# Performance work log

Measured on AMD Instinct MI355X. Metric: run time of the kernel, lower is better.

The kernel has to match this reference:

```python
import jax, jax.numpy as jnp
import numpy as np

EPS = 1e-6
HID = 2048; N_HEADS = 16; Q_LORA = 768; KV_LORA = 512
ROPE_D = 64; NOPE_D = 128; V_D = 128
IDX_H = 32; IDX_D = 128; IDX_TOPK = 512
N_EXP = 8; TOPK = 4; N_GROUP = 4; TOPK_GROUP = 2
MOE_I = 512; SHARED_I = 512; ROUTED_SCALE = 2.5
T = 1024
NEG = -1e30


def _rms(x, w, eps=EPS):
    x = x.astype(jnp.float32)
    return x * jax.lax.rsqrt(jnp.mean(x * x, axis=-1, keepdims=True) + eps) * w


def _ln(x, w, b, eps=EPS):
    x = x.astype(jnp.float32)
    m = jnp.mean(x, axis=-1, keepdims=True)
    v = jnp.mean((x - m) ** 2, axis=-1, keepdims=True)
    return (x - m) * jax.lax.rsqrt(v + eps) * w + b


def _rope_cs(positions, dim):
    inv = 1.0 / (10000.0 ** (jnp.arange(0, dim, 2, dtype=jnp.float32) / dim))
    f = positions.astype(jnp.float32)[:, None] * inv[None, :]  # [T, dim/2]
    return jnp.cos(f), jnp.sin(f)


def _rope(x, cos, sin):
    # neox-style rotate-half over last dim
    d = x.shape[-1] // 2
    x1, x2 = x[..., :d], x[..., d:]
    while cos.ndim < x.ndim:
        cos, sin = cos[:, None], sin[:, None]
    return jnp.concatenate([x1 * cos - x2 * sin, x2 * cos + x1 * sin], axis=-1)


def setup_inputs() -> dict:
    key = jax.random.key(0)
    ks = iter(jax.random.split(key, 32))
    w = lambda *s: jax.random.normal(next(ks), s, jnp.float32) * 0.02
    inp = {
        'positions': jnp.arange(T, dtype=jnp.int32),
        'hidden_states': jax.random.normal(next(ks), (T, HID), jnp.float32),
        'residual': jax.random.normal(next(ks), (T, HID), jnp.float32),
        'w_input_ln': jnp.ones((HID,), jnp.float32),
        'w_post_ln': jnp.ones((HID,), jnp.float32),
        'w_step1': w(Q_LORA + KV_LORA + ROPE_D + IDX_D + IDX_H, HID),
        'w_q_a_ln': jnp.ones((Q_LORA,), jnp.float32),
        'w_kv_a_ln': jnp.ones((KV_LORA,), jnp.float32),
        'idx_k_ln_w': jnp.ones((IDX_D,), jnp.float32),
        'idx_k_ln_b': jnp.zeros((IDX_D,), jnp.float32),
        'w_step3': w(IDX_H * IDX_D + N_HEADS * (NOPE_D + ROPE_D), Q_LORA),
        'W_UK_T': w(N_HEADS, NOPE_D, KV_LORA),
        'W_UV': w(N_HEADS, KV_LORA, V_D),
        'w_o': w(HID, N_HEADS * V_D),
        'gate_w': w(N_EXP, HID),
        'gate_bias': jnp.zeros((N_EXP,), jnp.float32),
        'shared_gate_up': w(2 * SHARED_I, HID),
        'shared_down': w(HID, SHARED_I),
        'exp_gate_up': w(N_EXP, 2 * MOE_I, HID),
        'exp_down': w(N_EXP, HID, MOE_I),
    }
    return inp


def reference(positions, hidden_states, residual, w_input_ln, w_post_ln, w_step1,
              w_q_a_ln, w_kv_a_ln, idx_k_ln_w, idx_k_ln_b, w_step3, W_UK_T, W_UV,
              w_o, gate_w, gate_bias, shared_gate_up, shared_down, exp_gate_up, exp_down):
    Tn = hidden_states.shape[0]
    rows = jnp.arange(Tn)
    # (allreduce is identity at tp=1) + residual add + RMSNorm
    res = hidden_states.astype(jnp.float32) + residual.astype(jnp.float32)
    h = _rms(res, w_input_ln)
    # ---- Step 1: fused qkv_a + indexer_wk + indexer_weights_proj GEMM ----
    s1 = h @ w_step1.T
    o0 = 0
    q_c = s1[:, o0:o0 + Q_LORA]; o0 += Q_LORA
    kv_c = s1[:, o0:o0 + KV_LORA]; o0 += KV_LORA
    k_pe = s1[:, o0:o0 + ROPE_D]; o0 += ROPE_D
    idx_k = s1[:, o0:o0 + IDX_D]; o0 += IDX_D
    idx_w_raw = s1[:, o0:o0 + IDX_H]
    cos, sin = _rope_cs(positions, ROPE_D)
    # fused_norm_rope: norms + rope on k_pe / indexer-k
    q_c = _rms(q_c, w_q_a_ln)
    kv_c = _rms(kv_c, w_kv_a_ln)
    k_pe = _rope(k_pe, cos, sin)
    idx_k = _ln(idx_k, idx_k_ln_w, idx_k_ln_b)
    idx_k = jnp.concatenate([_rope(idx_k[:, :ROPE_D], cos, sin), idx_k[:, ROPE_D:]], axis=-1)
    # ---- Step 3: fused indexer_wq_b + q_b_proj GEMM ----
    s3 = q_c @ w_step3.T
    idx_q = s3[:, :IDX_H * IDX_D].reshape(Tn, IDX_H, IDX_D)
    q = s3[:, IDX_H * IDX_D:].reshape(Tn, N_HEADS, NOPE_D + ROPE_D)
    q_nope, q_pe = q[..., :NOPE_D], q[..., NOPE_D:]
    # absorb W_UK: [T,H,nope] x [H,nope,kv_lora] -> [T,H,kv_lora]
    ql_nope = jnp.einsum('thn,hnk->thk', q_nope, W_UK_T)
    q_pe = _rope(q_pe, cos, sin)
    idx_q = jnp.concatenate([_rope(idx_q[..., :ROPE_D], cos, sin), idx_q[..., ROPE_D:]], axis=-1)
    idx_q = idx_q * (IDX_D ** -0.5)            # indexer softmax scale
    idx_w = idx_w_raw * (IDX_H ** -0.5)        # per-head weights scale
    # ---- sparse attention indexer: relu(q.k) head-weighted sum, causal top-k ----
    il = jnp.einsum('thd,sd->ths', idx_q, idx_k)          # [T,Hi,S]
    iscores = jnp.einsum('ths,th->ts', jax.nn.relu(il), idx_w)
    causal = positions[:, None] >= positions[None, :]
    iscores = jnp.where(causal, iscores, NEG)
    topk_idx = jax.lax.top_k(iscores, IDX_TOPK)[1]        # [T, IDX_TOPK]
    tmask = jnp.zeros((Tn, Tn), bool).at[rows[:, None], topk_idx].set(True)
    mask = causal & tmask
    # ---- MLA MQA attention in latent space ----
    mqa_q = jnp.concatenate([ql_nope, jnp.broadcast_to(q_pe, (Tn, N_HEADS, ROPE_D))], axis=-1)
    kv = jnp.concatenate([kv_c, k_pe], axis=-1)           # [S, kv_lora+rope]
    att = jnp.einsum('thd,sd->hts', mqa_q, kv) * ((NOPE_D + ROPE_D) ** -0.5)
    att = jnp.where(mask[None], att, NEG)
    p = jax.nn.softmax(att, axis=-1)
    o = jnp.einsum('hts,sk->thk', p, kv_c)                # [T,H,kv_lora]
    o = jnp.einsum('thk,hkv->thv', o, W_UV).reshape(Tn, N_HEADS * V_D)
    attn_out = o @ w_o.T
    # add + RMSNorm
    res2 = attn_out + res
    h2 = _rms(res2, w_post_ln)
    # ---- MoE: DeepSeekV3 sigmoid grouped routing + shared experts ----
    glog = h2 @ gate_w.T
    sg = jax.nn.sigmoid(glog)
    sc = sg + gate_bias
    gsz = N_EXP // N_GROUP
    grp = sc.reshape(Tn, N_GROUP, gsz)
    grp_score = jax.lax.top_k(grp, min(2, gsz))[0].sum(-1)
    gidx = jax.lax.top_k(grp_score, TOPK_GROUP)[1]
    gmask = jnp.zeros((Tn, N_GROUP), bool).at[rows[:, None], gidx].set(True)
    emask = jnp.repeat(gmask, gsz, axis=1)
    sc_m = jnp.where(emask, sc, NEG)
    _, tid = jax.lax.top_k(sc_m, TOPK)
    tw = jnp.take_along_axis(sg, tid, axis=1)
    tw = tw / (tw.sum(-1, keepdims=True) + 1e-20) * ROUTED_SCALE
    comb = jnp.zeros((Tn, N_EXP), jnp.float32).at[rows[:, None], tid].set(tw)
    # routed experts (dense masked combine as reference for grouped-GEMM dispatch)
    gu = jnp.einsum('th,eih->tei', h2, exp_gate_up)       # [T,E,2I]
    act = jax.nn.silu(gu[..., :MOE_I]) * gu[..., MOE_I:]
    routed_e = jnp.einsum('tei,ehi->teh', act, exp_down)  # [T,E,H]
    routed = jnp.einsum('te,teh->th', comb, routed_e)
    # shared experts
    gus = h2 @ shared_gate_up.T
    shared = (jax.nn.silu(gus[:, :SHARED_I]) * gus[:, SHARED_I:]) @ shared_down.T
    out = shared + routed
    return out, res2
```

## Files before the change

### kernel.cpp

```cpp
#include <hip/hip_runtime.h>
#include <math.h>

static constexpr int TT  = 1024;
static constexpr int HID = 2048;
static constexpr int NH  = 16;
static constexpr int QL  = 768;
static constexpr int KVL = 512;
static constexpr int RD  = 64;
static constexpr int IH  = 32;
static constexpr int ID  = 128;
static constexpr int S1W = QL + KVL + RD + ID + IH;
static constexpr int S3W = IH*ID + NH*(128+RD);

#define SCALE_ATT 0.07216878364870323f
#define SC_IDXQ   0.08838834764831845f
#define SC_IDXW   0.17677669529663687f
#define NEGR      -1e30f
#define NEGL      -3.0e38f

typedef __bf16 bf16x8 __attribute__((ext_vector_type(8)));
typedef float  f32x4  __attribute__((ext_vector_type(4)));

#define GLD_LDS16(g, l) __builtin_amdgcn_global_load_lds( \
    (const __attribute__((address_space(1))) void*)(g),   \
    (__attribute__((address_space(3))) void*)(l), 16, 0, 0)

__device__ __forceinline__ unsigned short f2b(float x) {
  union { float f; unsigned u; } v; v.f = x;
  unsigned r = v.u + 0x7FFFu + ((v.u >> 16) & 1u);
  return (unsigned short)(r >> 16);
}
__device__ __forceinline__ float b2f(unsigned short u) {
  union { unsigned u; float f; } v; v.u = ((unsigned)u) << 16;
  return v.f;
}

__device__ __forceinline__ float blk_sum256(float v, float* s) {
  #pragma unroll
  for (int o = 32; o > 0; o >>= 1) v += __shfl_down(v, o, 64);
  __syncthreads();
  if ((threadIdx.x & 63) == 0) s[threadIdx.x >> 6] = v;
  __syncthreads();
  return s[0] + s[1] + s[2] + s[3];
}

__global__ __launch_bounds__(256) void k_prelude(const float* __restrict__ hs,
                                                 const float* __restrict__ rsd,
                                                 const float* __restrict__ w,
                                                 float* __restrict__ res,
                                                 unsigned short* __restrict__ hb) {
  int t = blockIdx.x;
  __shared__ float scr[4];
  float vals[8]; float ss = 0.f;
  #pragma unroll
  for (int r = 0; r < 8; r++) {
    int d = threadIdx.x + 256*r;
    float v = hs[(size_t)t*HID + d] + rsd[(size_t)t*HID + d];
    vals[r] = v; res[(size_t)t*HID + d] = v; ss = fmaf(v, v, ss);
  }
  ss = blk_sum256(ss, scr);
  float inv = 1.f/sqrtf(ss/(float)HID + 1e-6f);
  #pragma unroll
  for (int r = 0; r < 8; r++) {
    int d = threadIdx.x + 256*r;
    hb[(size_t)t*HID + d] = f2b(vals[r]*inv*w[d]);
  }
}

__global__ __launch_bounds__(256) void k_res2(const float* __restrict__ attn1,
                                              const float* __restrict__ attn2,
                                              const float* __restrict__ res,
                                              const float* __restrict__ w,
                                              float* __restrict__ res2_out,
                                              float* __restrict__ h2,
                                              unsigned short* __restrict__ h2b) {
  int t = blockIdx.x;
  __shared__ float scr[4];
  float vals[8]; float ss = 0.f;
  #pragma unroll
  for (int r = 0; r < 8; r++) {
    int d = threadIdx.x + 256*r;
    float v = attn1[(size_t)t*HID + d] + attn2[(size_t)t*HID + d] + res[(size_t)t*HID + d];
    vals[r] = v; res2_out[(size_t)t*HID + d] = v; ss = fmaf(v, v, ss);
  }
  ss = blk_sum256(ss, scr);
  float inv = 1.f/sqrtf(ss/(float)HID + 1e-6f);
  #pragma unroll
  for (int r = 0; r < 8; r++) {
    int d = threadIdx.x + 256*r;
    float o = vals[r]*inv*w[d];
    h2[(size_t)t*HID + d] = o;
    h2b[(size_t)t*HID + d] = f2b(o);
  }
}

__global__ void k_ropecs(const int* __restrict__ pos, float* __restrict__ cosb, float* __restrict__ sinb) {
  int i = blockIdx.x*256 + threadIdx.x;
  if (i >= TT*32) return;
  int t = i >> 5, k = i & 31;
  double inv = pow(10000.0, -((double)(2*k))/64.0);
  double f = (double)pos[t] * inv;
  cosb[i] = (float)cos(f);
  sinb[i] = (float)sin(f);
}

__global__ void k_f2b(const float* __restrict__ s, unsigned short* __restrict__ d,
                      long long n, long long ntot) {
  long long stride = (long long)gridDim.x * 1024;
  for (long long i = ((long long)blockIdx.x*256 + threadIdx.x)*4; i < ntot; i += stride) {
    float x0, x1, x2, x3;
    if (i + 3 < n) { float4 v = *(const float4*)(s + i); x0=v.x; x1=v.y; x2=v.z; x3=v.w; }
    else {
      x0 = (i   < n) ? s[i]   : 0.f; x1 = (i+1 < n) ? s[i+1] : 0.f;
      x2 = (i+2 < n) ? s[i+2] : 0.f; x3 = (i+3 < n) ? s[i+3] : 0.f;
    }
    ushort4 o; o.x=f2b(x0); o.y=f2b(x1); o.z=f2b(x2); o.w=f2b(x3);
    *(ushort4*)(d + i) = o;
  }
}

__global__ void k_f2b4(const float* __restrict__ s0, unsigned short* __restrict__ d0, long long n0,
                       const float* __restrict__ s1, unsigned short* __restrict__ d1, long long n1,
                       const float* __restrict__ s2, unsigned short* __restrict__ d2, long long n2,
                       const float* __restrict__ s3, unsigned short* __restrict__ d3, long long n3) {
  long long ntot = n0 + n1 + n2 + n3;
  long long stride = (long long)gridDim.x * 1024;
  for (long long i = ((long long)blockIdx.x*256 + threadIdx.x)*4; i < ntot; i += stride) {
    const float* s; unsigned short* d; long long j = i;
    if (j < n0) { s = s0; d = d0; }
    else { j -= n0;
      if (j < n1) { s = s1; d = d1; }
      else { j -= n1;
        if (j < n2) { s = s2; d = d2; }
        else { j -= n2; s = s3; d = d3; } } }
    float4 v = *(const float4*)(s + j);
    ushort4 o; o.x=f2b(v.x); o.y=f2b(v.y); o.z=f2b(v.z); o.w=f2b(v.w);
    *(ushort4*)(d + j) = o;
  }
}

__global__ __launch_bounds__(256) void k_tconvb(const float* __restrict__ src,
                                                unsigned short* __restrict__ dst,
                                                int R, int C) {
  src += (size_t)blockIdx.z * R * C;
  dst += (size_t)blockIdx.z * R * C;
  __shared__ float tile[32][33];
  int c0 = blockIdx.x * 32, r0 = blockIdx.y * 32;
  int tx = threadIdx.x & 31, ty = threadIdx.x >> 5;
  #pragma unroll
  for (int i = 0; i < 4; i++) {
    int r = r0 + ty + i*8;
    tile[ty + i*8][tx] = src[(size_t)r*C + c0 + tx];
  }
  __syncthreads();
  #pragma unroll
  for (int i = 0; i < 4; i++) {
    int c = c0 + ty + i*8;
    dst[(size_t)c*R + r0 + tx] = f2b(tile[tx][ty + i*8]);
  }
}

template<int BM, int OUT, bool ILV, int MOE>
__global__ __launch_bounds__(256) void k_mgemm(
    const unsigned short* __restrict__ A, int lda, long long sA,
    const unsigned short* __restrict__ B, int ldb, long long sB,
    void* __restrict__ Cv, int ldc, long long sC,
    int N, int K, float alpha, int cskip, int ktri,
    int nseg, long long segA, long long segB,
    const float* __restrict__ comb,
    const int* __restrict__ cntp, const int* __restrict__ tokp) {
  constexpr int MR  = BM / 32;
  constexpr int ITA = BM / 32;
  const int row0 = blockIdx.y * BM;
  const int col0 = blockIdx.x * 128;
  const int tid  = threadIdx.x;
  if (cskip >= 0 && col0 > row0 + cskip) {
    if (OUT == 3) {
      float* C = (float*)Cv;
      for (int i = tid; i < BM*32; i += 256) {
        int rr = i >> 5, cc = (i & 31) * 4;
        float4 ng = make_float4(NEGR, NEGR, NEGR, NEGR);
        *(float4*)&C[(size_t)(row0 + rr)*ldc + col0 + cc] = ng;
      }
    }
    return;
  }
  const int zb = blockIdx.z;
  int cnt = 0; long long off = 0;
  if (MOE) {
    cnt = cntp[zb];
    for (int e = 0; e < zb; e++) off += cntp[e];
    if (row0 >= cnt) return;
  }
  __shared__ __align__(16) unsigned short As[2][BM*64];
  __shared__ __align__(16) unsigned short Bs[2][128*64];
  __shared__ float wlds[(OUT == 3) ? BM*32 : 1];
  const int wave = tid >> 6, lane = tid & 63;
  const int wm = wave >> 1, wn = wave & 1;
  A += (size_t)zb * (size_t)sA;
  B += (size_t)zb * (size_t)sB;
  if (MOE == 2) A += off * (long long)lda;

  if constexpr (OUT == 3) {
    for (int i = tid; i < BM*32; i += 256)
      wlds[i] = comb[(size_t)(row0 + (i >> 5))*32 + (i & 31)];
  }

  int tki[ITA];
  if (MOE == 1) {
    #pragma unroll
    for (int it = 0; it < ITA; it++) {
      int r = (wave*64 + it*256 + lane) >> 3;
      tki[it] = tokp[zb*1024 + row0 + r];
    }
  }

  f32x4 acc[MR][4] = {};
  f32x4 acc2[(OUT == 3) ? MR : 1][4] = {};
  const int l15 = lane & 15, l4 = lane >> 4;
  const int sx = l15 & 7;
  int Kend = K;
  if (ktri) {
    int kub = (((row0 + BM - 1) >> 7) + 1) << 7;
    if (kub < Kend) Kend = kub;
  }
  const int nk = Kend >> 6;
  const int nt = nseg * nk;

  auto STAGE = [&](int b, const unsigned short* Ab, const unsigned short* Bb, int k0) {
    #pragma unroll
    for (int it = 0; it < ITA; it++) {
      int base = wave*64 + it*256;
      int sidx = base + lane;
      int r = sidx >> 3, s = sidx & 7;
      int s_src = s ^ (r & 7);
      const unsigned short* ga;
      if (MOE == 1) ga = Ab + (size_t)tki[it]*lda + k0 + s_src*8;
      else          ga = Ab + (size_t)(row0 + r)*lda + k0 + s_src*8;
      GLD_LDS16(ga, &As[b][base*8]);
    }
    #pragma unroll
    for (int it = 0; it < 4; it++) {
      int base = wave*64 + it*256;
      int sidx = base + lane;
      int r = sidx >> 3, s = sidx & 7;
      int s_src = s ^ (r & 7);
      int rt = col0 + r;
      int srow = ILV ? ((rt >> 1) + (rt & 1)*512) : rt;
      const unsigned short* gb = Bb + (size_t)srow*ldb + k0 + s_src*8;
      GLD_LDS16(gb, &Bs[b][base*8]);
    }
  };

  STAGE(0, A, B, 0);
  int ks = 64, sg = 0;
  if (ks == Kend) { ks = 0; sg = 1; }
  __syncthreads();
  int cur = 0;

  for (int u = 0; u < nt; u++) {
    if (u + 1 < nt) {
      STAGE(cur ^ 1, A + (size_t)sg*segA, B + (size_t)sg*segB, ks);
      ks += 64;
      if (ks == Kend) { ks = 0; sg++; }
    }
    #pragma unroll
    for (int kc = 0; kc < 2; kc++) {
      const int sl = ((kc*4 + l4) ^ sx) << 3;
      bf16x8 fa[MR], fb[4];
      #pragma unroll
      for (int mf = 0; mf < MR; mf++)
        fa[mf] = *(const bf16x8*)&As[cur][(wm*(BM/2) + mf*16 + l15)*64 + sl];
      #pragma unroll
      for (int nf = 0; nf < 4; nf++)
        fb[nf] = *(const bf16x8*)&Bs[cur][(wn*64 + nf*16 + l15)*64 + sl];
      #pragma unroll
      for (int mf = 0; mf < MR; mf++)
        #pragma unroll
        for (int nf = 0; nf < 4; nf++)
          acc[mf][nf] = __builtin_amdgcn_mfma_f32_16x16x32_bf16(fa[mf], fb[nf], acc[mf][nf], 0, 0, 0);
    }
    if constexpr (OUT == 3) {
      if ((u + 1) % nk == 0) {
        int h = u / nk;
        #pragma unroll
        for (int mf = 0; mf < MR; mf++) {
          #pragma unroll
          for (int r = 0; r < 4; r++) {
            int rl = wm*(BM/2) + mf*16 + l4*4 + r;
            float w = wlds[rl*32 + h];
            #pragma unroll
            for (int nf = 0; nf < 4; nf++) {
              acc2[mf][nf][r] += fmaxf(acc[mf][nf][r], 0.f) * w;
              acc[mf][nf][r] = 0.f;
            }
          }
        }
      }
    }
    __syncthreads();
    cur ^= 1;
  }

  #pragma unroll
  for (int mf = 0; mf < MR; mf++) {
    #pragma unroll
    for (int nf = 0; nf < 4; nf++) {
      int n = col0 + wn*64 + nf*16 + l15;
      #pragma unroll
      for (int r = 0; r < 4; r++) {
        int m = row0 + wm*(BM/2) + mf*16 + l4*4 + r;
        if (OUT == 3) {
          float v = acc2[mf][nf][r];
          if (n > 512 + m) v = NEGR;
          ((float*)Cv)[(size_t)m*ldc + n] = v;
          continue;
        }
        float v = acc[mf][nf][r] * alpha;
        if (OUT == 2) {
          float p = __shfl_xor(v, 1, 64);
          if ((l15 & 1) == 0) {
            bool ok = true;
            long long mrow = m;
            float w;
            if (MOE == 1) {
              ok = (m < cnt); mrow = off + m;
              int tok = tokp[zb*1024 + m];
              w = (zb < 8) ? comb[tok*8 + zb] : 1.f;
            } else {
              w = (zb < 8) ? comb[m*8 + zb] : 1.f;
            }
            if (ok) {
              float rres = v/(1.f + expf(-v)) * p * w;
              ((unsigned short*)Cv)[(size_t)zb*sC + (size_t)mrow*ldc + (n >> 1)] = f2b(rres);
            }
          }
        } else if (n < N) {
          bool ok = true;
          long long mrow = m;
          if (MOE == 2) { ok = (m < cnt); mrow = off + m; }
          if (ok) {
            size_t idx = (size_t)mrow*ldc + n;
            if (OUT == 1) ((unsigned short*)Cv)[(size_t)zb*sC + idx] = f2b(v);
            else          ((float*)Cv)[(size_t)zb*sC + idx] = v;
          }
        }
      }
    }
  }
}

__global__ __launch_bounds__(256) void k_post1(const float* __restrict__ s1a,
    const float* __restrict__ s1b,
    const float* __restrict__ wq, const float* __restrict__ wkv,
    const float* __restrict__ lnw, const float* __restrict__ lnb,
    const float* __restrict__ cosb, const float* __restrict__ sinb,
    unsigned short* __restrict__ qcb, float* __restrict__ kvc, float* __restrict__ kpe,
    float* __restrict__ idxk, float* __restrict__ idxw) {
  int t = blockIdx.x, tid = threadIdx.x;
  __shared__ float rowb[S1W];
  __shared__ float scr[4];
  __shared__ float yb[128];
  for (int d = tid; d < S1W; d += 256)
    rowb[d] = s1a[(size_t)t*S1W + d] + s1b[(size_t)t*S1W + d];
  __syncthreads();
  float ss = 0.f;
  for (int d = tid; d < QL; d += 256) { float v = rowb[d]; ss = fmaf(v,v,ss); }
  ss = blk_sum256(ss, scr);
  float inv = 1.f/sqrtf(ss/(float)QL + 1e-6f);
  for (int d = tid; d < QL; d += 256) qcb[(size_t)t*QL + d] = f2b(rowb[d]*inv*wq[d]);
  ss = 0.f;
  for (int d = tid; d < KVL; d += 256) { float v = rowb[QL+d]; ss = fmaf(v,v,ss); }
  ss = blk_sum256(ss, scr);
  inv = 1.f/sqrtf(ss/(float)KVL + 1e-6f);
  for (int d = tid; d < KVL; d += 256) kvc[(size_t)t*KVL + d] = rowb[QL+d]*inv*wkv[d];
  float sm = (tid < 128) ? rowb[1344 + tid] : 0.f;
  float tot = blk_sum256(sm, scr);
  float mean = tot / 128.f;
  float vs = 0.f;
  if (tid < 128) { float v = rowb[1344+tid] - mean; vs = v*v; }
  vs = blk_sum256(vs, scr);
  float ivn = 1.f/sqrtf(vs/128.f + 1e-6f);
  if (tid < 128) yb[tid] = (rowb[1344+tid]-mean)*ivn*lnw[tid] + lnb[tid];
  __syncthreads();
  if (tid < 32) {
    float c = cosb[t*32 + tid], s = sinb[t*32 + tid];
    idxk[(size_t)t*ID + tid]      = yb[tid]*c - yb[32+tid]*s;
    idxk[(size_t)t*ID + 32 + tid] = yb[32+tid]*c + yb[tid]*s;
    float x1 = rowb[1280+tid], x2 = rowb[1312+tid];
    kpe[(size_t)t*RD + tid]      = x1*c - x2*s;
    kpe[(size_t)t*RD + 32 + tid] = x2*c + x1*s;
    idxw[(size_t)t*IH + tid] = rowb[1472+tid] * SC_IDXW;
  } else if (tid >= 64 && tid < 128) {
    idxk[(size_t)t*ID + tid] = yb[tid];
  }
}

__global__ __launch_bounds__(256) void k_post3b(const float* __restrict__ s3,
                                                const float* __restrict__ cosb,
                                                const float* __restrict__ sinb,
                                                unsigned short* __restrict__ s3b) {
  int t = blockIdx.x, tid = threadIdx.x;
  const float* row = s3 + (size_t)t*S3W;
  __shared__ float buf[S3W];
  __shared__ float cs[32], sn[32];
  if (tid < 32) { cs[tid] = cosb[t*32+tid]; sn[tid] = sinb[t*32+tid]; }
  for (int d = tid; d < S3W; d += 256) buf[d] = row[d];
  __syncthreads();
  for (int p = tid; p < 1024; p += 256) {
    int h = p >> 5, d = p & 31;
    float c = cs[d], s = sn[d];
    float x1 = buf[h*ID + d], x2 = buf[h*ID + 32 + d];
    buf[h*ID + d]      = (x1*c - x2*s) * SC_IDXQ;
    buf[h*ID + 32 + d] = (x2*c + x1*s) * SC_IDXQ;
  }
  for (int p = tid; p < 2048; p += 256) {
    int h = p >> 6, d = 64 + (p & 63);
    buf[h*ID + d] *= SC_IDXQ;
  }
  for (int p = tid; p < 512; p += 256) {
    int h = p >> 5, d = p & 31;
    float c = cs[d], s = sn[d];
    int base = IH*ID + h*192 + 128;
    float x1 = buf[base + d], x2 = buf[base + 32 + d];
    buf[base + d]      = x1*c - x2*s;
    buf[base + 32 + d] = x2*c + x1*s;
  }
  __syncthreads();
  unsigned short* orow = s3b + (size_t)t*S3W;
  for (int g = tid*4; g < S3W; g += 1024) {
    ushort4 o;
    o.x = f2b(buf[g]); o.y = f2b(buf[g+1]); o.z = f2b(buf[g+2]); o.w = f2b(buf[g+3]);
    *(ushort4*)(orow + g) = o;
  }
}

__global__ void k_qpe(const unsigned short* __restrict__ s3b, unsigned short* __restrict__ qm) {
  int i = blockIdx.x*256 + threadIdx.x;
  int t = i >> 10, r = i & 1023;
  int h = r >> 6, j = r & 63;
  float v = b2f(s3b[(size_t)t*S3W + IH*ID + h*192 + 128 + j]) * SCALE_ATT;
  qm[(size_t)t*9216 + h*576 + 512 + j] = f2b(v);
}

__global__ void k_kvb(const float* __restrict__ kvc, const float* __restrict__ kpe,
                      unsigned short* __restrict__ kvb) {
  int i = blockIdx.x*256 + threadIdx.x;
  int s = i / 576, d = i - s*576;
  float v = (d < 512) ? kvc[(size_t)s*KVL + d] : kpe[(size_t)s*RD + (d - 512)];
  kvb[i] = f2b(v);
}

__global__ __launch_bounds__(512) void k_topk(const float* __restrict__ isc,
                                              unsigned char* __restrict__ mask) {
  int t = 512 + blockIdx.x;
  const float* row = isc + (size_t)blockIdx.x * TT;
  __shared__ unsigned long long keys[1024];
  int tid = threadIdx.x;
  for (int i = tid; i < 1024; i += 512) {
    float v = row[i];
    unsigned int b = __float_as_uint(v);
    unsigned int u = (b & 0x80000000u) ? ~b : (b | 0x80000000u);
    keys[i] = ((unsigned long long)u << 32) | (unsigned int)(1023 - i);
  }
  __syncthreads();
  for (int k = 2; k <= 1024; k <<= 1) {
    for (int j = k >> 1; j > 0; j >>= 1) {
      int i = ((tid & ~(j - 1)) << 1) | (tid & (j - 1));
      int l = i | j;
      unsigned long long a = keys[i], b = keys[l];
      bool up = ((i & k) == 0);
      if ((a < b) == up) { keys[i] = b; keys[l] = a; }
      __syncthreads();
    }
  }
  unsigned char* mrow = mask + (size_t)t * TT;
  for (int p = tid; p < 1024; p += 512) {
    int s = 1023 - (int)(keys[p] & 0xFFFFFFFFu);
    mrow[s] = (p < 512) ? (unsigned char)1 : (unsigned char)0;
  }
}

__global__ __launch_bounds__(256) void k_psoft(unsigned short* __restrict__ pb,
                                               const unsigned char* __restrict__ mask) {
  int b = blockIdx.x;
  int t = b & 1023, h = b >> 10;
  unsigned short* row = pb + ((size_t)h << 20) + ((size_t)t << 10);
  int tid = threadIdx.x;
  __shared__ float scr[4];
  int s0 = tid * 4;
  int rub = ((t >> 7) + 1) << 7;
  bool act = (s0 < rub);
  float v0 = 0.f, v1 = 0.f, v2 = 0.f, v3 = 0.f;
  bool m0 = false, m1 = false, m2 = false, m3 = false;
  if (act) {
    ushort4 raw = *(const ushort4*)(row + s0);
    v0 = b2f(raw.x); v1 = b2f(raw.y); v2 = b2f(raw.z); v3 = b2f(raw.w);
    if (t < 512) {
      m0 = (s0 <= t); m1 = (s0+1 <= t); m2 = (s0+2 <= t); m3 = (s0+3 <= t);
    } else {
      uchar4 mk = *(const uchar4*)(mask + (size_t)t*TT + s0);
      m0 = (s0 <= t) && mk.x; m1 = (s0+1 <= t) && mk.y;
      m2 = (s0+2 <= t) && mk.z; m3 = (s0+3 <= t) && mk.w;
    }
  }
  float mx = NEGL;
  if (m0) mx = v0;
  if (m1) mx = fmaxf(mx, v1);
  if (m2) mx = fmaxf(mx, v2);
  if (m3) mx = fmaxf(mx, v3);
  #pragma unroll
  for (int o = 32; o > 0; o >>= 1) mx = fmaxf(mx, __shfl_down(mx, o, 64));
  __syncthreads();
  if ((tid & 63) == 0) scr[tid >> 6] = mx;
  __syncthreads();
  mx = fmaxf(fmaxf(scr[0], scr[1]), fmaxf(scr[2], scr[3]));
  float p0 = m0 ? expf(v0 - mx) : 0.f;
  float p1 = m1 ? expf(v1 - mx) : 0.f;
  float p2 = m2 ? expf(v2 - mx) : 0.f;
  float p3 = m3 ? expf(v3 - mx) : 0.f;
  float sum = blk_sum256((p0+p1)+(p2+p3), scr);
  float inv = 1.f / sum;
  if (act) {
    ushort4 o;
    o.x = f2b(p0*inv); o.y = f2b(p1*inv); o.z = f2b(p2*inv); o.w = f2b(p3*inv);
    *(ushort4*)(row + s0) = o;
  }
}

__global__ __launch_bounds__(256) void k_gate(const float* __restrict__ h2,
                                              const float* __restrict__ gw,
                                              const float* __restrict__ gb,
                                              float* __restrict__ comb) {
  int t = blockIdx.x, tid = threadIdx.x;
  int e = tid >> 5, lane = tid & 31;
  __shared__ float gl[8];
  float p = 0.f;
  for (int d = lane; d < HID; d += 32) p = fmaf(h2[(size_t)t*HID+d], gw[(size_t)e*HID+d], p);
  #pragma unroll
  for (int o = 16; o > 0; o >>= 1) p += __shfl_down(p, o, 32);
  if (lane == 0) gl[e] = p;
  __syncthreads();
  if (tid == 0) {
    float sg[8], sc[8];
    #pragma unroll
    for (int i = 0; i < 8; i++) { sg[i] = 1.f/(1.f+expf(-gl[i])); sc[i] = sg[i] + gb[i]; }
    float gs[4];
    #pragma unroll
    for (int g = 0; g < 4; g++) gs[g] = sc[2*g] + sc[2*g+1];
    int g0 = 0;
    for (int g = 1; g < 4; g++) if (gs[g] > gs[g0]) g0 = g;
    int g1 = -1;
    for (int g = 0; g < 4; g++) { if (g == g0) continue; if (g1 < 0 || gs[g] > gs[g1]) g1 = g; }
    float wsum = 1e-20f;
    #pragma unroll
    for (int i = 0; i < 8; i++) { int g = i >> 1; if (g == g0 || g == g1) wsum += sg[i]; }
    #pragma unroll
    for (int i = 0; i < 8; i++) { int g = i >> 1; comb[t*8+i] = (g == g0 || g == g1) ? sg[i]/wsum*2.5f : 0.f; }
  }
}

__global__ __launch_bounds__(1024) void k_route(const float* __restrict__ comb,
                                                int* __restrict__ tokidx,
                                                int* __restrict__ rank,
                                                int* __restrict__ cntp) {
  int e = blockIdx.x;
  int t = threadIdx.x;
  if (e == 8) {
    tokidx[8*1024 + t] = t;
    if (t == 0) cntp[8] = 1024;
    return;
  }
  int lane = t & 63, w = t >> 6;
  bool sel = comb[t*8 + e] != 0.0f;
  unsigned long long bal = __ballot(sel);
  int pw = __popcll(bal & ((1ull << lane) - 1ull));
  int wt = __popcll(bal);
  __shared__ int wsum[16];
  if (lane == 0) wsum[w] = wt;
  __syncthreads();
  int woff = 0, total = 0;
  #pragma unroll
  for (int i = 0; i < 16; i++) { int v = wsum[i]; if (i < w) woff += v; total += v; }
  int pos = woff + pw;
  rank[t*8 + e] = sel ? pos : -1;
  if (sel) tokidx[e*1024 + pos] = t;
  __syncthreads();
  if (t >= total) tokidx[e*1024 + t] = 0;
  if (t == 0) cntp[e] = total;
}

__global__ __launch_bounds__(256) void k_rsum(const unsigned short* __restrict__ dpc,
                                              const int* __restrict__ rank,
                                              const int* __restrict__ cntp,
                                              float* __restrict__ out) {
  int t = blockIdx.x;
  int d = threadIdx.x * 8;
  int offs[8]; int acc_off = 0;
  #pragma unroll
  for (int e = 0; e < 8; e++) { offs[e] = acc_off; acc_off += cntp[e]; }
  const unsigned short* ps = dpc + (size_t)(acc_off + t)*2048 + d;
  ushort4 u0 = *(const ushort4*)ps;
  ushort4 u1 = *(const ushort4*)(ps + 4);
  float a[8];
  a[0]=b2f(u0.x); a[1]=b2f(u0.y); a[2]=b2f(u0.z); a[3]=b2f(u0.w);
  a[4]=b2f(u1.x); a[5]=b2f(u1.y); a[6]=b2f(u1.z); a[7]=b2f(u1.w);
  #pragma unroll
  for (int e = 0; e < 8; e++) {
    int r = rank[t*8 + e];
    if (r >= 0) {
      const unsigned short* p = dpc + (size_t)(offs[e] + r)*2048 + d;
      ushort4 b0 = *(const ushort4*)p;
      ushort4 b1 = *(const ushort4*)(p + 4);
      a[0]+=b2f(b0.x); a[1]+=b2f(b0.y); a[2]+=b2f(b0.z); a[3]+=b2f(b0.w);
      a[4]+=b2f(b1.x); a[5]+=b2f(b1.y); a[6]+=b2f(b1.z); a[7]+=b2f(b1.w);
    }
  }
  float* po = out + (size_t)t*2048 + d;
  *(float4*)po       = make_float4(a[0], a[1], a[2], a[3]);
  *(float4*)(po + 4) = make_float4(a[4], a[5], a[6], a[7]);
}

extern "C" void kernel_launch(void* const* d_in, const int* in_sizes, int n_in,
                              void* d_out, int out_size, void* d_ws, size_t ws_size,
                              hipStream_t stream) {
  const int*   positions = (const int*)d_in[0];
  const float* hs     = (const float*)d_in[1];
  const float* rsd    = (const float*)d_in[2];
  const float* w_in   = (const float*)d_in[3];
  const float* w_post = (const float*)d_in[4];
  const float* w_s1   = (const float*)d_in[5];
  const float* w_qln  = (const float*)d_in[6];
  const float* w_kvln = (const float*)d_in[7];
  const float* iklnw  = (const float*)d_in[8];
  const float* iklnb  = (const float*)d_in[9];
  const float* w_s3   = (const float*)d_in[10];
  const float* wukt   = (const float*)d_in[11];
  const float* wuv    = (const float*)d_in[12];
  const float* w_o    = (const float*)d_in[13];
  const float* gate_w = (const float*)d_in[14];
  const float* gate_b = (const float*)d_in[15];
  const float* sh_gu  = (const float*)d_in[16];
  const float* sh_dn  = (const float*)d_in[17];
  const float* ex_gu  = (const float*)d_in[18];
  const float* ex_dn  = (const float*)d_in[19];

  float* ws = (float*)d_ws;
  typedef unsigned short ush;
  float* RES   = ws + 0;
  float* COSB  = ws + 2097152;
  float* SINB  = ws + 2129920;
  float* KVC   = ws + 2162688;
  float* KPE   = ws + 2686976;
  float* IDXK  = ws + 2752512;
  float* IDXW  = ws + 2883584;
  float* COMB  = ws + 2916352;
  ush*   HB    = (ush*)(ws + 2924544);
  ush*   WS1B  = (ush*)(ws + 3973120);
  float* S1P0  = ws + 5545984;
  ush*   QCB   = (ush*)(ws + 7086080);
  ush*   WS3B  = (ush*)(ws + 7479296);
  ush*   WOB   = (ush*)(ws + 7479296);
  float* S3    = ws + 10231808;
  float* S1P1  = ws + 10231808;
  ush*   S3B   = (ush*)(ws + 17571840);
  ush*   WUKTB = (ush*)(ws + 21241856);
  ush*   QMQAB = (ush*)(ws + 21766144);
  float* ISC   = ws + 26484736;
  unsigned char* MASK = (unsigned char*)(ws + 27009024);
  ush*   WUVB  = (ush*)(ws + 27271168);
  ush*   KVB   = (ush*)(ws + 27795456);
  ush*   VTB   = (ush*)(ws + 28090368);
  ush*   O2B   = (ush*)(ws + 28352512);
  ush*   IDXKB = (ush*)(ws + 31989760);
  ush*   PB    = (ush*)(ws + 10231808);
  ush*   OHB   = (ush*)(ws + 18620416);
  float* ATTNP = ws + 10231808;
  float* H2     = ws + 2924544;
  ush*   H2B    = (ush*)(ws + 5021696);
  ush*   EXGUB  = (ush*)(ws + 6070272);
  ush*   SHGUB  = (ush*)(ws + 14458880);
  ush*   EXDNB  = (ush*)(ws + 15507456);
  ush*   SHDNB  = (ush*)(ws + 19701760);
  ush*   ACTC   = (ush*)(ws + 20226048);
  ush*   DPC    = (ush*)(ws + 21536768);
  int*   TOKIDX = (int*)(ws + 32022528);
  int*   RANK   = (int*)(ws + 32031744);
  int*   CNT    = (int*)(ws + 32039936);

  float* OUT0 = (float*)d_out;
  float* OUT_RES2 = OUT0 + (size_t)TT*HID;

  k_prelude<<<TT, 256, 0, stream>>>(hs, rsd, w_in, RES, HB);
  k_ropecs<<<(TT*32)/256, 256, 0, stream>>>(positions, COSB, SINB);
  k_f2b<<<1024, 256, 0, stream>>>(w_s1, WS1B, 3080192LL, 3145728LL);
  k_f2b<<<1024, 256, 0, stream>>>(w_s3, WS3B, 5505024LL, 5505024LL);
  k_tconvb<<<dim3(16,4,16), 256, 0, stream>>>(wukt, WUKTB, 128, 512);
  k_tconvb<<<dim3(4,16,16), 256, 0, stream>>>(wuv, WUVB, 512, 128);
  k_mgemm<128,0,false,0><<<dim3(12,8,2), 256, 0, stream>>>(
      HB, 2048, 1024, WS1B, 2048, 1024, S1P0, S1W, 4685824,
      1504, 1024, 1.f, -1, 0, 1, 0, 0, nullptr, nullptr, nullptr);
  k_post1<<<TT, 256, 0, stream>>>(S1P0, S1P1, w_qln, w_kvln, iklnw, iklnb, COSB, SINB, QCB, KVC, KPE, IDXK, IDXW);
  k_f2b<<<128, 256, 0, stream>>>(IDXK, IDXKB, 131072LL, 131072LL);
  k_mgemm<128,0,false,0><<<dim3(56,8,1), 256, 0, stream>>>(
      QCB, 768, 0, WS3B, 768, 0, S3, S3W, 0,
      S3W, 768, 1.f, -1, 0, 1, 0, 0, nullptr, nullptr, nullptr);
  k_post3b<<<TT, 256, 0, stream>>>(S3, COSB, SINB, (ush*)S3B);
  k_f2b<<<1024, 256, 0, stream>>>(w_o, WOB, 4194304LL, 4194304LL);
  k_mgemm<128,1,false,0><<<dim3(4,8,16), 256, 0, stream>>>(
      S3B + 4096, S3W, 192, WUKTB, 128, 65536, QMQAB, 9216, 576,
      512, 128, SCALE_ATT, -1, 0, 1, 0, 0, nullptr, nullptr, nullptr);
  k_qpe<<<4096, 256, 0, stream>>>(S3B, QMQAB);
  k_mgemm<64,3,false,0><<<dim3(8,8,1), 256, 0, stream>>>(
      S3B + (size_t)512*S3W, S3W, 0, IDXKB, 128, 0,
      ISC, 1024, 0, 1024, 128, 1.f, 575, 0, 32, 128, 0,
      IDXW + (size_t)512*IH, nullptr, nullptr);
  k_topk<<<512, 512, 0, stream>>>(ISC, MASK);
  k_kvb<<<2304, 256, 0, stream>>>(KVC, KPE, KVB);
  k_tconvb<<<dim3(16,32,1), 256, 0, stream>>>(KVC, VTB, 1024, 512);
  k_mgemm<128,1,false,0><<<dim3(8,8,16), 256, 0, stream>>>(
      QMQAB, 9216, 576, KVB, 576, 0, PB, 1024, 1048576,
      1024, 576, 1.f, 127, 0, 1, 0, 0, nullptr, nullptr, nullptr);
  k_psoft<<<16384, 256, 0, stream>>>(PB, MASK);
  k_mgemm<128,1,false,0><<<dim3(4,8,16), 256, 0, stream>>>(
      PB, 1024, 1048576, VTB, 1024, 0, OHB, 512, 524288,
      512, 1024, 1.f, -1, 1, 1, 0, 0, nullptr, nullptr, nullptr);
  k_mgemm<128,1,false,0><<<dim3(1,8,16), 256, 0, stream>>>(
      OHB, 512, 524288, WUVB, 512, 65536, O2B, 2048, 128,
      128, 512, 1.f, -1, 0, 1, 0, 0, nullptr, nullptr, nullptr);
  k_mgemm<128,0,false,0><<<dim3(16,8,2), 256, 0, stream>>>(
      O2B, 2048, 1024, WOB, 2048, 1024, ATTNP, 2048, 2097152,
      2048, 1024, 1.f, -1, 0, 1, 0, 0, nullptr, nullptr, nullptr);
  k_res2<<<TT, 256, 0, stream>>>(ATTNP, ATTNP + 2097152, RES, w_post, OUT_RES2, H2, H2B);
  k_gate<<<TT, 256, 0, stream>>>(H2, gate_w, gate_b, COMB);
  k_route<<<9, 1024, 0, stream>>>(COMB, TOKIDX, RANK, CNT);
  k_f2b4<<<2048, 256, 0, stream>>>(ex_gu, EXGUB, 16777216LL,
                                   sh_gu, SHGUB, 2097152LL,
                                   ex_dn, EXDNB, 8388608LL,
                                   sh_dn, SHDNB, 1048576LL);
  k_mgemm<128,2,true,1><<<dim3(8,8,9), 256, 0, stream>>>(
      H2B, 2048, 0, EXGUB, 2048, 2097152, ACTC, 512, 0,
      1024, 2048, 1.f, -1, 0, 1, 0, 0, COMB, CNT, TOKIDX);
  k_mgemm<128,1,false,2><<<dim3(16,8,9), 256, 0, stream>>>(
      ACTC, 512, 0, EXDNB, 512, 1048576, DPC, 2048, 0,
      2048, 512, 1.f, -1, 0, 1, 0, 0, nullptr, CNT, nullptr);
  k_rsum<<<TT, 256, 0, stream>>>(DPC, RANK, CNT, OUT0);
}
```

Baseline: 426.9 us.

## Deepen GEMM prefetch pipeline and fuse bf16 pack kernels into post-processing

```diff
diff --git a/kernel.cpp b/kernel.cpp
--- a/kernel.cpp
+++ b/kernel.cpp
@@ -24,6 +24,22 @@
 #define GLD_LDS16(g, l) __builtin_amdgcn_global_load_lds( \
     (const __attribute__((address_space(1))) void*)(g),   \
     (__attribute__((address_space(3))) void*)(l), 16, 0, 0)
+
+__device__ __forceinline__ void pipe_barrier() {
+  __builtin_amdgcn_sched_barrier(0);
+  asm volatile("" ::: "memory");
+  __builtin_amdgcn_s_barrier();
+  asm volatile("" ::: "memory");
+  __builtin_amdgcn_sched_barrier(0);
+}
+__device__ __forceinline__ void wait_vm8() {
+  asm volatile("s_waitcnt vmcnt(8)" ::: "memory");
+  __builtin_amdgcn_sched_barrier(0);
+}
+__device__ __forceinline__ void wait_vm0() {
+  asm volatile("s_waitcnt vmcnt(0)" ::: "memory");
+  __builtin_amdgcn_sched_barrier(0);
+}
 
 __device__ __forceinline__ unsigned short f2b(float x) {
   union { float f; unsigned u; } v; v.f = x;
@@ -254,16 +270,18 @@
 
   STAGE(0, A, B, 0);
   int ks = 64, sg = 0;
-  if (ks == Kend) { ks = 0; sg = 1; }
-  __syncthreads();
-  int cur = 0;
+  if (ks == Kend) { ks = 0; sg++; }
+  if (nt > 1) {
+    STAGE(1, A + (size_t)sg*segA, B + (size_t)sg*segB, ks);
+    ks += 64; if (ks == Kend) { ks = 0; sg++; }
+    wait_vm8();
+  } else {
+    wait_vm0();
+  }
+  pipe_barrier();
 
   for (int u = 0; u < nt; u++) {
-    if (u + 1 < nt) {
-      STAGE(cur ^ 1, A + (size_t)sg*segA, B + (size_t)sg*segB, ks);
-      ks += 64;
-      if (ks == Kend) { ks = 0; sg++; }
-    }
+    const int cur = u & 1;
     #pragma unroll
     for (int kc = 0; kc < 2; kc++) {
       const int sl = ((kc*4 + l4) ^ sx) << 3;
@@ -298,8 +316,17 @@
         }
       }
     }
-    __syncthreads();
-    cur ^= 1;
+    pipe_barrier();
+    if (u + 1 < nt) {
+      if (u + 2 < nt) {
+        STAGE(cur, A + (size_t)sg*segA, B + (size_t)sg*segB, ks);
+        ks += 64; if (ks == Kend) { ks = 0; sg++; }
+        wait_vm8();
+      } else {
+        wait_vm0();
+      }
+      pipe_barrier();
+    }
   }
 
   #pragma unroll
@@ -355,8 +382,9 @@
     const float* __restrict__ wq, const float* __restrict__ wkv,
     const float* __restrict__ lnw, const float* __restrict__ lnb,
     const float* __restrict__ cosb, const float* __restrict__ sinb,
-    unsigned short* __restrict__ qcb, float* __restrict__ kvc, float* __restrict__ kpe,
-    float* __restrict__ idxk, float* __restrict__ idxw) {
+    unsigned short* __restrict__ qcb, float* __restrict__ kvc,
+    unsigned short* __restrict__ kvb, unsigned short* __restrict__ idxkb,
+    float* __restrict__ idxw) {
   int t = blockIdx.x, tid = threadIdx.x;
   __shared__ float rowb[S1W];
   __shared__ float scr[4];
@@ -373,7 +401,11 @@
   for (int d = tid; d < KVL; d += 256) { float v = rowb[QL+d]; ss = fmaf(v,v,ss); }
   ss = blk_sum256(ss, scr);
   inv = 1.f/sqrtf(ss/(float)KVL + 1e-6f);
-  for (int d = tid; d < KVL; d += 256) kvc[(size_t)t*KVL + d] = rowb[QL+d]*inv*wkv[d];
+  for (int d = tid; d < KVL; d += 256) {
+    float v = rowb[QL+d]*inv*wkv[d];
+    kvc[(size_t)t*KVL + d] = v;
+    kvb[(size_t)t*576 + d] = f2b(v);
+  }
   float sm = (tid < 128) ? rowb[1344 + tid] : 0.f;
   float tot = blk_sum256(sm, scr);
   float mean = tot / 128.f;
@@ -385,21 +417,22 @@
   __syncthreads();
   if (tid < 32) {
     float c = cosb[t*32 + tid], s = sinb[t*32 + tid];
-    idxk[(size_t)t*ID + tid]      = yb[tid]*c - yb[32+tid]*s;
-    idxk[(size_t)t*ID + 32 + tid] = yb[32+tid]*c + yb[tid]*s;
+    idxkb[(size_t)t*ID + tid]      = f2b(yb[tid]*c - yb[32+tid]*s);
+    idxkb[(size_t)t*ID + 32 + tid] = f2b(yb[32+tid]*c + yb[tid]*s);
     float x1 = rowb[1280+tid], x2 = rowb[1312+tid];
-    kpe[(size_t)t*RD + tid]      = x1*c - x2*s;
-    kpe[(size_t)t*RD + 32 + tid] = x2*c + x1*s;
+    kvb[(size_t)t*576 + 512 + tid] = f2b(x1*c - x2*s);
+    kvb[(size_t)t*576 + 544 + tid] = f2b(x2*c + x1*s);
     idxw[(size_t)t*IH + tid] = rowb[1472+tid] * SC_IDXW;
   } else if (tid >= 64 && tid < 128) {
-    idxk[(size_t)t*ID + tid] = yb[tid];
+    idxkb[(size_t)t*ID + tid] = f2b(yb[tid]);
   }
 }
 
 __global__ __launch_bounds__(256) void k_post3b(const float* __restrict__ s3,
                                                 const float* __restrict__ cosb,
                                                 const float* __restrict__ sinb,
-                                                unsigned short* __restrict__ s3b) {
+                                                unsigned short* __restrict__ s3b,
+                                                unsigned short* __restrict__ qm) {
   int t = blockIdx.x, tid = threadIdx.x;
   const float* row = s3 + (size_t)t*S3W;
   __shared__ float buf[S3W];
@@ -423,8 +456,11 @@
     float c = cs[d], s = sn[d];
     int base = IH*ID + h*192 + 128;
     float x1 = buf[base + d], x2 = buf[base + 32 + d];
-    buf[base + d]      = x1*c - x2*s;
-    buf[base + 32 + d] = x2*c + x1*s;
+    float r1 = x1*c - x2*s, r2 = x2*c + x1*s;
+    buf[base + d]      = r1;
+    buf[base + 32 + d] = r2;
+    qm[(size_t)t*9216 + h*576 + 512 + d]      = f2b(r1 * SCALE_ATT);
+    qm[(size_t)t*9216 + h*576 + 544 + d]      = f2b(r2 * SCALE_ATT);
   }
   __syncthreads();
   unsigned short* orow = s3b + (size_t)t*S3W;
@@ -433,22 +469,6 @@
     o.x = f2b(buf[g]); o.y = f2b(buf[g+1]); o.z = f2b(buf[g+2]); o.w = f2b(buf[g+3]);
     *(ushort4*)(orow + g) = o;
   }
-}
-
-__global__ void k_qpe(const unsigned short* __restrict__ s3b, unsigned short* __restrict__ qm) {
-  int i = blockIdx.x*256 + threadIdx.x;
-  int t = i >> 10, r = i & 1023;
-  int h = r >> 6, j = r & 63;
-  float v = b2f(s3b[(size_t)t*S3W + IH*ID + h*192 + 128 + j]) * SCALE_ATT;
-  qm[(size_t)t*9216 + h*576 + 512 + j] = f2b(v);
-}
-
-__global__ void k_kvb(const float* __restrict__ kvc, const float* __restrict__ kpe,
-                      unsigned short* __restrict__ kvb) {
-  int i = blockIdx.x*256 + threadIdx.x;
-  int s = i / 576, d = i - s*576;
-  float v = (d < 512) ? kvc[(size_t)s*KVL + d] : kpe[(size_t)s*RD + (d - 512)];
-  kvb[i] = f2b(v);
 }
 
 __global__ __launch_bounds__(512) void k_topk(const float* __restrict__ isc,
@@ -651,8 +671,6 @@
   float* COSB  = ws + 2097152;
   float* SINB  = ws + 2129920;
   float* KVC   = ws + 2162688;
-  float* KPE   = ws + 2686976;
-  float* IDXK  = ws + 2752512;
   float* IDXW  = ws + 2883584;
   float* COMB  = ws + 2916352;
   ush*   HB    = (ush*)(ws + 2924544);
@@ -700,23 +718,21 @@
   k_mgemm<128,0,false,0><<<dim3(12,8,2), 256, 0, stream>>>(
       HB, 2048, 1024, WS1B, 2048, 1024, S1P0, S1W, 4685824,
       1504, 1024, 1.f, -1, 0, 1, 0, 0, nullptr, nullptr, nullptr);
-  k_post1<<<TT, 256, 0, stream>>>(S1P0, S1P1, w_qln, w_kvln, iklnw, iklnb, COSB, SINB, QCB, KVC, KPE, IDXK, IDXW);
-  k_f2b<<<128, 256, 0, stream>>>(IDXK, IDXKB, 131072LL, 131072LL);
+  k_post1<<<TT, 256, 0, stream>>>(S1P0, S1P1, w_qln, w_kvln, iklnw, iklnb, COSB, SINB,
+                                  QCB, KVC, KVB, IDXKB, IDXW);
   k_mgemm<128,0,false,0><<<dim3(56,8,1), 256, 0, stream>>>(
       QCB, 768, 0, WS3B, 768, 0, S3, S3W, 0,
       S3W, 768, 1.f, -1, 0, 1, 0, 0, nullptr, nullptr, nullptr);
-  k_post3b<<<TT, 256, 0, stream>>>(S3, COSB, SINB, (ush*)S3B);
+  k_post3b<<<TT, 256, 0, stream>>>(S3, COSB, SINB, (ush*)S3B, QMQAB);
   k_f2b<<<1024, 256, 0, stream>>>(w_o, WOB, 4194304LL, 4194304LL);
   k_mgemm<128,1,false,0><<<dim3(4,8,16), 256, 0, stream>>>(
       S3B + 4096, S3W, 192, WUKTB, 128, 65536, QMQAB, 9216, 576,
       512, 128, SCALE_ATT, -1, 0, 1, 0, 0, nullptr, nullptr, nullptr);
-  k_qpe<<<4096, 256, 0, stream>>>(S3B, QMQAB);
   k_mgemm<64,3,false,0><<<dim3(8,8,1), 256, 0, stream>>>(
       S3B + (size_t)512*S3W, S3W, 0, IDXKB, 128, 0,
       ISC, 1024, 0, 1024, 128, 1.f, 575, 0, 32, 128, 0,
       IDXW + (size_t)512*IH, nullptr, nullptr);
   k_topk<<<512, 512, 0, stream>>>(ISC, MASK);
-  k_kvb<<<2304, 256, 0, stream>>>(KVC, KPE, KVB);
   k_tconvb<<<dim3(16,32,1), 256, 0, stream>>>(KVC, VTB, 1024, 512);
   k_mgemm<128,1,false,0><<<dim3(8,8,16), 256, 0, stream>>>(
       QMQAB, 9216, 576, KVB, 576, 0, PB, 1024, 1048576,
```

New measurement: 459.5 us. 7.6% more time.
